# Kernel tuning notes

Hardware: AMD Instinct MI355X
Metric: run time of the kernel (lower is better)

The kernel has to match this reference:

```python
import jax, jax.numpy as jnp
import numpy as np

D = 256
HEADS = 8
LEVELS = 4
POINTS = 4
HD = D // HEADS  # 32
SHAPES = [(96, 96), (48, 48), (24, 24), (12, 12)]
N_BATCH = 2


def setup_inputs() -> dict:
    key = jax.random.key(0)
    ks = jax.random.split(key, 10)
    Lin = sum(h * w for h, w in SHAPES)  # 12240
    src = jax.random.normal(ks[0], (N_BATCH, Lin, D), jnp.float32)
    reference_points = jax.random.uniform(ks[1], (N_BATCH, Lin, LEVELS, 2), jnp.float32)
    spatial_shapes = np.array(SHAPES, dtype=np.int64)
    level_start_index = np.concatenate([[0], np.cumsum([h * w for h, w in SHAPES])[:-1]]).astype(np.int64)
    s = 0.02
    w_value = s * jax.random.normal(ks[2], (D, D), jnp.float32)
    b_value = jnp.zeros((D,), jnp.float32)
    w_off = s * jax.random.normal(ks[3], (D, HEADS * LEVELS * POINTS * 2), jnp.float32)
    b_off = 0.5 * jax.random.normal(ks[4], (HEADS * LEVELS * POINTS * 2,), jnp.float32)
    w_attn = s * jax.random.normal(ks[5], (D, HEADS * LEVELS * POINTS), jnp.float32)
    b_attn = jnp.zeros((HEADS * LEVELS * POINTS,), jnp.float32)
    w_out = s * jax.random.normal(ks[6], (D, D), jnp.float32)
    b_out = jnp.zeros((D,), jnp.float32)
    gamma = jnp.ones((D,), jnp.float32)
    beta = jnp.zeros((D,), jnp.float32)
    return dict(src=src, reference_points=reference_points, spatial_shapes=spatial_shapes,
                level_start_index=level_start_index, w_value=w_value, b_value=b_value,
                w_off=w_off, b_off=b_off, w_attn=w_attn, b_attn=b_attn,
                w_out=w_out, b_out=b_out, gamma=gamma, beta=beta)


def _bilinear_sample(value_flat, H, W, loc):
    # value_flat: (N, heads, H*W, hd); loc: (N, heads, Lq, P, 2) normalized [0,1]
    # Equivalent to F.grid_sample(bilinear, padding_mode='zeros', align_corners=False)
    x = loc[..., 0] * W - 0.5
    y = loc[..., 1] * H - 0.5
    x0 = jnp.floor(x)
    y0 = jnp.floor(y)
    lx = x - x0
    ly = y - y0
    n, h, Lq, P = x.shape
    out = jnp.zeros((n, h, Lq, P, value_flat.shape[-1]), value_flat.dtype)
    for dy, wy in ((0, 1.0 - ly), (1, ly)):
        for dx, wx in ((0, 1.0 - lx), (1, lx)):
            xi = x0 + dx
            yi = y0 + dy
            valid = (xi >= 0) & (xi < W) & (yi >= 0) & (yi < H)
            idx = (jnp.clip(yi, 0, H - 1) * W + jnp.clip(xi, 0, W - 1)).astype(jnp.int32)
            v = jnp.take_along_axis(value_flat, idx.reshape(n, h, Lq * P, 1), axis=2)
            v = v.reshape(n, h, Lq, P, -1)
            out = out + v * (wx * wy * valid.astype(value_flat.dtype))[..., None]
    return out


def reference(src, reference_points, spatial_shapes, level_start_index,
              w_value, b_value, w_off, b_off, w_attn, b_attn, w_out, b_out, gamma, beta):
    N, Lq, _ = src.shape
    shapes = np.asarray(spatial_shapes)
    starts = np.asarray(level_start_index)

    # projections
    value = (src @ w_value + b_value).reshape(N, Lq, HEADS, HD)
    offsets = (src @ w_off + b_off).reshape(N, Lq, HEADS, LEVELS, POINTS, 2)
    attn = (src @ w_attn + b_attn).reshape(N, Lq, HEADS, LEVELS * POINTS)
    attn = jax.nn.softmax(attn, axis=-1).reshape(N, Lq, HEADS, LEVELS, POINTS)

    # sampling locations: ref + offset / (W_l, H_l)
    normalizer = jnp.asarray(shapes[:, ::-1].copy(), jnp.float32)  # (L, 2) = (W, H)
    loc = reference_points[:, :, None, :, None, :] + offsets / normalizer[None, None, None, :, None, :]

    out = jnp.zeros((N, HEADS, Lq, HD), src.dtype)
    for l in range(LEVELS):
        H, W = int(shapes[l, 0]), int(shapes[l, 1])
        s0 = int(starts[l])
        v_l = value[:, s0:s0 + H * W].transpose(0, 2, 1, 3)        # (N, heads, HW, hd)
        loc_l = loc[:, :, :, l].transpose(0, 2, 1, 3, 4)           # (N, heads, Lq, P, 2)
        sampled = _bilinear_sample(v_l, H, W, loc_l)               # (N, heads, Lq, P, hd)
        w_l = attn[:, :, :, l].transpose(0, 2, 1, 3)               # (N, heads, Lq, P)
        out = out + (sampled * w_l[..., None]).sum(axis=3)
    out = out.transpose(0, 2, 1, 3).reshape(N, Lq, D)
    out = out @ w_out + b_out

    # residual (dropout in eval = identity) + LayerNorm
    x = src + out
    mu = x.mean(-1, keepdims=True)
    var = x.var(-1, keepdims=True)
    return (x - mu) / jnp.sqrt(var + 1e-5) * gamma + beta
```

## Files before the change

### kernel.cpp

```cpp
#include <hip/hip_runtime.h>
#include <cstdint>
#include <cstddef>

#define D 256
#define HEADS 8
#define HD 32
#define NB 2
#define LQ 12240
#define NQ (NB * LQ)
#define PLANE (LQ * HD)

typedef __attribute__((ext_vector_type(8))) short bf16x8;
typedef __attribute__((ext_vector_type(4))) float f32x4;
typedef __bf16 bf16x2 __attribute__((ext_vector_type(2)));

__device__ __forceinline__ ushort f2bf(float f) {
    union { float f; uint32_t u; } c; c.f = f;
    uint32_t u = c.u;
    uint32_t r = (u + 0x7fffu + ((u >> 16) & 1u)) >> 16;
    return (ushort)r;
}
__device__ __forceinline__ float bflo(uint32_t u) { return __uint_as_float(u << 16); }
__device__ __forceinline__ float bfhi(uint32_t u) { return __uint_as_float(u & 0xffff0000u); }

__device__ __forceinline__ float dot2bf(uint32_t a, uint32_t b, float c) {
#if __has_builtin(__builtin_amdgcn_fdot2_f32_bf16)
    return __builtin_amdgcn_fdot2_f32_bf16(__builtin_bit_cast(bf16x2, a),
                                           __builtin_bit_cast(bf16x2, b), c, false);
#else
    return c + bflo(a) * bflo(b) + bfhi(a) * bfhi(b);
#endif
}

__global__ __launch_bounds__(256) void conv_kernel(
    const float* __restrict__ w_value, const float* __restrict__ w_off,
    const float* __restrict__ w_attn,  const float* __restrict__ b_value,
    const float* __restrict__ b_off,   const float* __restrict__ b_attn,
    const float* __restrict__ w_out,   const float* __restrict__ src,
    ushort* __restrict__ B_pack, ushort* __restrict__ w_out_t,
    float* __restrict__ b_pack, ushort* __restrict__ src_bf)
{
    const int b = blockIdx.x, k = threadIdx.x;
    if (b >= 899) {
        const size_t i = ((size_t)(b - 899) * 256 + k) * 4;
        float4 v = *(const float4*)(src + i);
        ushort4 o;
        o.x = f2bf(v.x); o.y = f2bf(v.y); o.z = f2bf(v.z); o.w = f2bf(v.w);
        *(ushort4*)(src_bf + i) = o;
        return;
    }
    if (b < 640) {
        float v;
        if (b < 256)      v = w_value[(size_t)k * 256 + b];
        else if (b < 512) v = w_off[(size_t)k * 256 + (b - 256)];
        else              v = w_attn[(size_t)k * 128 + (b - 512)];
        B_pack[(size_t)b * 256 + k] = f2bf(v);
    } else if (b < 896) {
        int n = b - 640;
        w_out_t[(size_t)n * 256 + k] = f2bf(w_out[(size_t)k * 256 + n]);
    } else if (b == 896) {
        b_pack[k] = b_value[k];
    } else if (b == 897) {
        b_pack[256 + k] = b_off[k];
    } else {
        if (k < 128) b_pack[512 + k] = b_attn[k];
    }
}

__global__ __launch_bounds__(256, 2) void proj_gemm(
    const ushort* __restrict__ src_bf, const ushort* __restrict__ B_pack,
    const float* __restrict__ b_pack,
    ushort* __restrict__ val_t, float* __restrict__ off_raw,
    float* __restrict__ attn_raw)
{
    const int tid = threadIdx.x;
    const int wv = tid >> 6, lane = tid & 63;
    const int quad = lane >> 4, ln = lane & 15;
    const int mc = blockIdx.x;
    const int by = blockIdx.y;

    const ushort* bp = B_pack + (size_t)(by * 64 + ln) * 256 + quad * 8;
    bf16x8 bfr[4][8];
#pragma unroll
    for (int t = 0; t < 4; ++t)
#pragma unroll
        for (int s = 0; s < 8; ++s)
            bfr[t][s] = *(const bf16x8*)(bp + (size_t)t * (16 * 256) + s * 32);

    float bias[4];
#pragma unroll
    for (int t = 0; t < 4; ++t) bias[t] = b_pack[by * 64 + t * 16 + ln];

    for (int i = 0; i < 6; ++i) {
        const int base = (mc * 6 + i) * 64;
        if (base >= NQ) break;
        const int row_a = base + wv * 16 + ln;
        const bool va = row_a < NQ;
        const ushort* ap = src_bf + (size_t)row_a * 256 + quad * 8;

        bf16x8 af[8];
#pragma unroll
        for (int s = 0; s < 8; ++s) {
            bf16x8 v = {0, 0, 0, 0, 0, 0, 0, 0};
            if (va) v = *(const bf16x8*)(ap + s * 32);
            af[s] = v;
        }

        f32x4 acc[4] = {{0,0,0,0},{0,0,0,0},{0,0,0,0},{0,0,0,0}};
#pragma unroll
        for (int s = 0; s < 8; ++s)
#pragma unroll
            for (int t = 0; t < 4; ++t)
                acc[t] = __builtin_amdgcn_mfma_f32_16x16x32_bf16(af[s], bfr[t][s], acc[t], 0, 0, 0);

        if (by < 4) {
#pragma unroll
            for (int t = 0; t < 4; ++t) {
                const int n_g = by * 64 + t * 16 + ln;
                const int h = n_g >> 5, hd = n_g & 31;
#pragma unroll
                for (int reg = 0; reg < 4; ++reg) {
                    int row = base + wv * 16 + quad * 4 + reg;
                    if (row < NQ) {
                        int nb = row >= LQ; int ql = row - nb * LQ;
                        val_t[(((size_t)(nb * 8 + h)) * LQ + ql) * 32 + hd] =
                            f2bf(acc[t][reg] + bias[t]);
                    }
                }
            }
        } else if (by < 8) {
#pragma unroll
            for (int t = 0; t < 4; ++t) {
                const int col = (by - 4) * 64 + t * 16 + ln;
#pragma unroll
                for (int reg = 0; reg < 4; ++reg) {
                    int row = base + wv * 16 + quad * 4 + reg;
                    if (row < NQ)
                        off_raw[(size_t)row * 256 + col] = acc[t][reg] + bias[t];
                }
            }
        } else {
#pragma unroll
            for (int t = 0; t < 4; ++t) {
                const int col = (by - 8) * 64 + t * 16 + ln;
#pragma unroll
                for (int reg = 0; reg < 4; ++reg) {
                    int row = base + wv * 16 + quad * 4 + reg;
                    if (row < NQ)
                        attn_raw[(size_t)row * 128 + col] = acc[t][reg] + bias[t];
                }
            }
        }
    }
}

__global__ __launch_bounds__(256) void pair_kernel(
    const ushort* __restrict__ val_t, uint32_t* __restrict__ val_pair)
{
    const uint32_t i = blockIdx.x * 256 + threadIdx.x;
    const uint32_t c = i & 31;
    const uint32_t rest = i >> 5;
    const uint32_t plane = rest / LQ;
    const uint32_t pos = rest - plane * LQ;
    int l = (pos >= 9216) + (pos >= 11520) + (pos >= 12096);
    uint32_t s0 = (l > 0 ? 9216u : 0u) + (l > 1 ? 2304u : 0u) + (l > 2 ? 576u : 0u);
    uint32_t Wi = 96u >> l;
    uint32_t p = pos - s0;
    uint32_t q = (p / 3u) >> (5 - l);
    uint32_t xr = p - q * Wi;
    uint32_t nxt = (xr == Wi - 1u) ? pos : pos + 1u;
    uint32_t lo = val_t[(size_t)plane * PLANE + pos * 32 + c];
    uint32_t hi = val_t[(size_t)plane * PLANE + nxt * 32 + c];
    val_pair[i] = lo | (hi << 16);
}

__global__ __launch_bounds__(256) void sample_kernel(
    const float* __restrict__ ref_pts,
    const uint32_t* __restrict__ val_pair,
    const float* __restrict__ off_raw,
    const float* attn_raw,
    uint32_t* sampled)
{
    __shared__ uint32_t sm_i[16][2][18];
    __shared__ uint32_t sm_w[16][2][18];
    const int gl = threadIdx.x >> 4;
    const int ln = threadIdx.x & 15;
    const int h     = blockIdx.x & 7;
    const int chunk = blockIdx.x >> 3;
    const int qg = chunk * 16 + gl;
    const int n  = (qg >= LQ) ? 1 : 0;
    const int l  = ln >> 2;

    float a = attn_raw[(size_t)qg * 128 + h * 16 + ln];
    float m = a;
#pragma unroll
    for (int s = 8; s; s >>= 1) m = fmaxf(m, __shfl_xor(m, s, 16));
    float e = __expf(a - m);
    float ssum = e;
#pragma unroll
    for (int s = 8; s; s >>= 1) ssum += __shfl_xor(ssum, s, 16);
    float aw = e / ssum;

    float ox = off_raw[(size_t)qg * 256 + h * 32 + ln * 2 + 0];
    float oy = off_raw[(size_t)qg * 256 + h * 32 + ln * 2 + 1];
    float rx = ref_pts[(qg * 4 + l) * 2 + 0];
    float ry = ref_pts[(qg * 4 + l) * 2 + 1];

    const int Wi = 96 >> l;
    const int Hi = Wi;
    const int s0 = (l > 0 ? 9216 : 0) + (l > 1 ? 2304 : 0) + (l > 2 ? 576 : 0);
    const float Wf = (float)Wi, Hf = (float)Hi;

    float x = (rx + ox / Wf) * Wf - 0.5f;
    float y = (ry + oy / Hf) * Hf - 0.5f;
    float x0f = floorf(x), y0f = floorf(y);
    float lx = x - x0f, ly = y - y0f;
    int x0 = (int)x0f, y0 = (int)y0f;

    float wy0 = (y0 >= 0 && y0 < Hi) ? (1.f - ly) : 0.f;
    float wy1 = (y0 + 1 >= 0 && y0 + 1 < Hi) ? ly : 0.f;
    int yc0 = min(max(y0, 0), Hi - 1);
    int yc1 = min(max(y0 + 1, 0), Hi - 1);
    float wl = (x0 >= 0 && x0 < Wi) ? (1.f - lx) : 0.f;
    float wh = (x0 + 1 >= 0 && x0 + 1 < Wi) ? lx : 0.f;
    float pl, ph;
    int xe;
    if (x0 < 0) { pl = wh; ph = 0.f; xe = x0 + 1; }
    else        { pl = wl; ph = wh;  xe = x0; }
    int xc = min(max(xe, 0), Wi - 1);
    pl *= aw; ph *= aw;

    sm_i[gl][0][ln] = (uint32_t)(s0 + yc0 * Wi + xc) * 32u;
    sm_i[gl][1][ln] = (uint32_t)(s0 + yc1 * Wi + xc) * 32u;
    sm_w[gl][0][ln] = ((uint32_t)f2bf(ph * wy0) << 16) | (uint32_t)f2bf(pl * wy0);
    sm_w[gl][1][ln] = ((uint32_t)f2bf(ph * wy1) << 16) | (uint32_t)f2bf(pl * wy1);

    const int half = ln >> 3;
    const int cb   = (ln & 7) * 4;
    const uint32_t* plane =
        val_pair + (size_t)(n * HEADS + h) * PLANE + cb;

    float a0 = 0.f, a1 = 0.f, a2 = 0.f, a3 = 0.f;
#pragma unroll
    for (int c = 0; c < 2; ++c) {
        uint4    rv[8];
        uint32_t wpk[8];
#pragma unroll
        for (int p = 0; p < 8; ++p) {
            uint32_t off = sm_i[gl][half][c * 8 + p];
            rv[p]  = *(const uint4*)(plane + off);
            wpk[p] = sm_w[gl][half][c * 8 + p];
        }
#pragma unroll
        for (int p = 0; p < 8; ++p) {
            a0 = dot2bf(rv[p].x, wpk[p], a0);
            a1 = dot2bf(rv[p].y, wpk[p], a1);
            a2 = dot2bf(rv[p].z, wpk[p], a2);
            a3 = dot2bf(rv[p].w, wpk[p], a3);
        }
    }
    a0 += __shfl_xor(a0, 8, 16);
    a1 += __shfl_xor(a1, 8, 16);
    a2 += __shfl_xor(a2, 8, 16);
    a3 += __shfl_xor(a3, 8, 16);
    if (ln < 8) {
        uint2 rr;
        rr.x = ((uint32_t)f2bf(a1) << 16) | (uint32_t)f2bf(a0);
        rr.y = ((uint32_t)f2bf(a3) << 16) | (uint32_t)f2bf(a2);
        *(uint2*)(sampled + (size_t)qg * 128 + h * 16 + 2 * ln) = rr;
    }
}

__global__ __launch_bounds__(256, 2) void out_ln_gemm(
    const ushort* __restrict__ sampled, const ushort* __restrict__ w_out_t,
    const float* __restrict__ b_out,    const float* __restrict__ src,
    const float* __restrict__ gamma,    const float* __restrict__ beta,
    float* __restrict__ out)
{
    __shared__ float sm_gb[3][256];
    const int tid = threadIdx.x;
    sm_gb[0][tid] = gamma[tid];
    sm_gb[1][tid] = beta[tid];
    sm_gb[2][tid] = b_out[tid];
    __syncthreads();

    const int wv = tid >> 6, lane = tid & 63;
    const int quad = lane >> 4, ln = lane & 15;
    const int base = blockIdx.x * 64;
    const int row_a = base + wv * 16 + ln;
    const bool va = row_a < NQ;
    const ushort* ap = sampled + (size_t)row_a * 256 + quad * 8;

    f32x4 acc[16];
#pragma unroll
    for (int t = 0; t < 16; ++t) acc[t] = (f32x4){0.f, 0.f, 0.f, 0.f};

#pragma unroll
    for (int sh = 0; sh < 2; ++sh) {
        bf16x8 af[4];
#pragma unroll
        for (int s = 0; s < 4; ++s) {
            bf16x8 v = {0, 0, 0, 0, 0, 0, 0, 0};
            if (va) v = *(const bf16x8*)(ap + (sh * 4 + s) * 32);
            af[s] = v;
        }
#pragma unroll
        for (int s = 0; s < 4; ++s) {
            const ushort* bp = w_out_t + (size_t)ln * 256 + quad * 8 + (sh * 4 + s) * 32;
#pragma unroll
            for (int t = 0; t < 16; ++t) {
                bf16x8 bf = *(const bf16x8*)(bp + (size_t)t * (16 * 256));
                acc[t] = __builtin_amdgcn_mfma_f32_16x16x32_bf16(af[s], bf, acc[t], 0, 0, 0);
            }
        }
    }

#pragma unroll
    for (int reg = 0; reg < 4; ++reg) {
        const int row = base + wv * 16 + quad * 4 + reg;
        const bool vr = row < NQ;
        float s1 = 0.f, s2 = 0.f;
        if (vr) {
            const float* sp = src + (size_t)row * 256 + ln;
#pragma unroll
            for (int t = 0; t < 16; ++t) {
                float v = acc[t][reg] + sm_gb[2][t * 16 + ln] + sp[t * 16];
                acc[t][reg] = v;
                s1 += v; s2 += v * v;
            }
        }
#pragma unroll
        for (int o = 8; o; o >>= 1) {
            s1 += __shfl_xor(s1, o, 16);
            s2 += __shfl_xor(s2, o, 16);
        }
        float mu  = s1 * (1.f / 256.f);
        float var = s2 * (1.f / 256.f) - mu * mu;
        float rs  = rsqrtf(var + 1e-5f);
        if (vr) {
            float* op = out + (size_t)row * 256 + ln;
#pragma unroll
            for (int t = 0; t < 16; ++t)
                op[t * 16] = (acc[t][reg] - mu) * rs * sm_gb[0][t * 16 + ln]
                           + sm_gb[1][t * 16 + ln];
        }
    }
}

extern "C" void kernel_launch(void* const* d_in, const int* in_sizes, int n_in,
                              void* d_out, int out_size, void* d_ws, size_t ws_size,
                              hipStream_t stream)
{
    const float* src     = (const float*)d_in[0];
    const float* refp    = (const float*)d_in[1];
    const float* w_value = (const float*)d_in[4];
    const float* b_value = (const float*)d_in[5];
    const float* w_off   = (const float*)d_in[6];
    const float* b_off   = (const float*)d_in[7];
    const float* w_attn  = (const float*)d_in[8];
    const float* b_attn  = (const float*)d_in[9];
    const float* w_out   = (const float*)d_in[10];
    const float* b_out   = (const float*)d_in[11];
    const float* gamma   = (const float*)d_in[12];
    const float* beta    = (const float*)d_in[13];

    char* ws = (char*)d_ws;
    ushort*   val_t    = (ushort*)  (ws);
    uint32_t* val_pair = (uint32_t*)(ws + 12533760);
    ushort*   src_bf   = (ushort*)  (ws + 12533760);
    float*    off_raw  = (float*)   (ws + 37601280);
    float*    attn_raw = (float*)   (ws + 62668800);
    uint32_t* sampled  = (uint32_t*)(ws + 62668800);
    ushort*   B_pack   = (ushort*)  (ws + 75202560);
    ushort*   w_out_t  = (ushort*)  (ws + 75530240);
    float*    b_pack   = (float*)   (ws + 75661312);
    float*    out      = (float*)d_out;

    conv_kernel<<<7019, 256, 0, stream>>>(w_value, w_off, w_attn, b_value, b_off,
                                          b_attn, w_out, src, B_pack, w_out_t,
                                          b_pack, src_bf);
    proj_gemm<<<dim3(64, 10), 256, 0, stream>>>(src_bf, B_pack, b_pack, val_t,
                                                off_raw, attn_raw);
    pair_kernel<<<24480, 256, 0, stream>>>(val_t, val_pair);
    sample_kernel<<<12240, 256, 0, stream>>>(refp, val_pair, off_raw, attn_raw,
                                             sampled);
    out_ln_gemm<<<383, 256, 0, stream>>>((const ushort*)sampled, w_out_t,
                                         b_out, src, gamma, beta, out);
}
```

Baseline: 215.1 us.

## Restructure output GEMM+LayerNorm so waves split columns with register-resident weights

The output projection plus LayerNorm kernel now assigns each wave a 64-column slice of the output and keeps that wave's slice of w_out in registers for the whole block. Each block processes three 16-row tiles in sequence and prefetches the next tile's activations while the current tile is reduced. Per-row LayerNorm statistics are combined across waves through double-buffered shared memory with a barrier per tile. The intent is to stop every wave re-reading the full weight matrix from global memory. The cost is higher register pressure and extra synchronisation, and the grid of 510 blocks covers exactly NQ rows, so the row bounds checks were removed.

```diff
diff --git a/kernel.cpp b/kernel.cpp
--- a/kernel.cpp
+++ b/kernel.cpp
@@ -277,73 +277,95 @@
     const float* __restrict__ gamma,    const float* __restrict__ beta,
     float* __restrict__ out)
 {
-    __shared__ float sm_gb[3][256];
+    __shared__ float sm[2][4][16][2];
     const int tid = threadIdx.x;
-    sm_gb[0][tid] = gamma[tid];
-    sm_gb[1][tid] = beta[tid];
-    sm_gb[2][tid] = b_out[tid];
-    __syncthreads();
-
     const int wv = tid >> 6, lane = tid & 63;
     const int quad = lane >> 4, ln = lane & 15;
-    const int base = blockIdx.x * 64;
-    const int row_a = base + wv * 16 + ln;
-    const bool va = row_a < NQ;
-    const ushort* ap = sampled + (size_t)row_a * 256 + quad * 8;
-
-    f32x4 acc[16];
-#pragma unroll
-    for (int t = 0; t < 16; ++t) acc[t] = (f32x4){0.f, 0.f, 0.f, 0.f};
-
-#pragma unroll
-    for (int sh = 0; sh < 2; ++sh) {
-        bf16x8 af[4];
-#pragma unroll
-        for (int s = 0; s < 4; ++s) {
-            bf16x8 v = {0, 0, 0, 0, 0, 0, 0, 0};
-            if (va) v = *(const bf16x8*)(ap + (sh * 4 + s) * 32);
-            af[s] = v;
-        }
-#pragma unroll
-        for (int s = 0; s < 4; ++s) {
-            const ushort* bp = w_out_t + (size_t)ln * 256 + quad * 8 + (sh * 4 + s) * 32;
-#pragma unroll
-            for (int t = 0; t < 16; ++t) {
-                bf16x8 bf = *(const bf16x8*)(bp + (size_t)t * (16 * 256));
-                acc[t] = __builtin_amdgcn_mfma_f32_16x16x32_bf16(af[s], bf, acc[t], 0, 0, 0);
-            }
-        }
-    }
-
-#pragma unroll
-    for (int reg = 0; reg < 4; ++reg) {
-        const int row = base + wv * 16 + quad * 4 + reg;
-        const bool vr = row < NQ;
-        float s1 = 0.f, s2 = 0.f;
-        if (vr) {
-            const float* sp = src + (size_t)row * 256 + ln;
-#pragma unroll
-            for (int t = 0; t < 16; ++t) {
-                float v = acc[t][reg] + sm_gb[2][t * 16 + ln] + sp[t * 16];
+
+    const ushort* bp = w_out_t + (size_t)(wv * 64 + ln) * 256 + quad * 8;
+    bf16x8 bfr[4][8];
+#pragma unroll
+    for (int t = 0; t < 4; ++t)
+#pragma unroll
+        for (int s = 0; s < 8; ++s)
+            bfr[t][s] = *(const bf16x8*)(bp + (size_t)t * (16 * 256) + s * 32);
+
+    float bias[4], gam[4], bet[4];
+#pragma unroll
+    for (int t = 0; t < 4; ++t) {
+        const int col = wv * 64 + t * 16 + ln;
+        bias[t] = b_out[col];
+        gam[t]  = gamma[col];
+        bet[t]  = beta[col];
+    }
+
+    int base = blockIdx.x * 48;
+
+    bf16x8 af[8];
+    {
+        const ushort* ap = sampled + (size_t)(base + ln) * 256 + quad * 8;
+#pragma unroll
+        for (int s = 0; s < 8; ++s) af[s] = *(const bf16x8*)(ap + s * 32);
+    }
+
+    for (int i = 0; i < 3; ++i) {
+        f32x4 acc[4] = {{0,0,0,0},{0,0,0,0},{0,0,0,0},{0,0,0,0}};
+#pragma unroll
+        for (int s = 0; s < 8; ++s)
+#pragma unroll
+            for (int t = 0; t < 4; ++t)
+                acc[t] = __builtin_amdgcn_mfma_f32_16x16x32_bf16(af[s], bfr[t][s], acc[t], 0, 0, 0);
+
+        bf16x8 afn[8];
+        if (i < 2) {
+            const ushort* apn = sampled + (size_t)(base + 16 + ln) * 256 + quad * 8;
+#pragma unroll
+            for (int s = 0; s < 8; ++s) afn[s] = *(const bf16x8*)(apn + s * 32);
+        }
+
+#pragma unroll
+        for (int reg = 0; reg < 4; ++reg) {
+            const int row = base + quad * 4 + reg;
+            const float* sp = src + (size_t)row * 256 + wv * 64 + ln;
+            float s1 = 0.f, s2 = 0.f;
+#pragma unroll
+            for (int t = 0; t < 4; ++t) {
+                float v = acc[t][reg] + bias[t] + sp[t * 16];
                 acc[t][reg] = v;
                 s1 += v; s2 += v * v;
             }
-        }
-#pragma unroll
-        for (int o = 8; o; o >>= 1) {
-            s1 += __shfl_xor(s1, o, 16);
-            s2 += __shfl_xor(s2, o, 16);
-        }
-        float mu  = s1 * (1.f / 256.f);
-        float var = s2 * (1.f / 256.f) - mu * mu;
-        float rs  = rsqrtf(var + 1e-5f);
-        if (vr) {
-            float* op = out + (size_t)row * 256 + ln;
-#pragma unroll
-            for (int t = 0; t < 16; ++t)
-                op[t * 16] = (acc[t][reg] - mu) * rs * sm_gb[0][t * 16 + ln]
-                           + sm_gb[1][t * 16 + ln];
-        }
+#pragma unroll
+            for (int o = 8; o; o >>= 1) {
+                s1 += __shfl_xor(s1, o, 16);
+                s2 += __shfl_xor(s2, o, 16);
+            }
+            if (ln == 0) {
+                sm[i & 1][wv][quad * 4 + reg][0] = s1;
+                sm[i & 1][wv][quad * 4 + reg][1] = s2;
+            }
+        }
+        __syncthreads();
+
+#pragma unroll
+        for (int reg = 0; reg < 4; ++reg) {
+            const int r16 = quad * 4 + reg;
+            float s1 = sm[i & 1][0][r16][0] + sm[i & 1][1][r16][0]
+                     + sm[i & 1][2][r16][0] + sm[i & 1][3][r16][0];
+            float s2 = sm[i & 1][0][r16][1] + sm[i & 1][1][r16][1]
+                     + sm[i & 1][2][r16][1] + sm[i & 1][3][r16][1];
+            float mu  = s1 * (1.f / 256.f);
+            float var = s2 * (1.f / 256.f) - mu * mu;
+            float rs  = rsqrtf(var + 1e-5f);
+            const int row = base + quad * 4 + reg;
+            float* op = out + (size_t)row * 256 + wv * 64 + ln;
+#pragma unroll
+            for (int t = 0; t < 4; ++t)
+                op[t * 16] = (acc[t][reg] - mu) * rs * gam[t] + bet[t];
+        }
+
+        base += 16;
+#pragma unroll
+        for (int s = 0; s < 8; ++s) af[s] = afn[s];
     }
 }
 
@@ -384,6 +406,6 @@
     pair_kernel<<<24480, 256, 0, stream>>>(val_t, val_pair);
     sample_kernel<<<12240, 256, 0, stream>>>(refp, val_pair, off_raw, attn_raw,
                                              sampled);
-    out_ln_gemm<<<383, 256, 0, stream>>>((const ushort*)sampled, w_out_t,
+    out_ln_gemm<<<510, 256, 0, stream>>>((const ushort*)sampled, w_out_t,
                                          b_out, src, gamma, beta, out);
 }
```

Measured after the change: 198.5 us. -7.7%, faster.
